# Optimization experiments

Measured on AMD Instinct MI355X. Metric: run time of the kernel, lower is better.

The kernel has to match this reference:

```python
import jax, jax.numpy as jnp
import numpy as np

B, S, E = 2, 2048, 1024
N_HEADS = 16
HEAD_DIM = E // N_HEADS  # 64
ATTN_SCALE = 1.0 / np.sqrt(E)  # NOTE: original scales by 1/sqrt(hidden_dim_phi), not head_dim
ROPE_BASE = 10000.0


def _rope(t):
    # t: (B, H, S, D) with D = HEAD_DIM; interleaved-pair RoPE (torchtune-style)
    d = t.shape[-1]
    s = t.shape[-2]
    inv_freq = 1.0 / (ROPE_BASE ** (jnp.arange(0, d, 2, dtype=jnp.float32) / d))  # (D/2,)
    ang = jnp.arange(s, dtype=jnp.float32)[:, None] * inv_freq[None, :]  # (S, D/2)
    cos, sin = jnp.cos(ang), jnp.sin(ang)  # (S, D/2)
    tp = t.reshape(t.shape[:-1] + (d // 2, 2))
    te, to = tp[..., 0], tp[..., 1]  # (B,H,S,D/2)
    oe = te * cos - to * sin
    oo = te * sin + to * cos
    return jnp.stack([oe, oo], axis=-1).reshape(t.shape)


def setup_inputs() -> dict:
    key = jax.random.key(0)
    ks = jax.random.split(key, 5)
    std = 0.02
    return {
        "x": jax.random.normal(ks[0], (B, S, E), dtype=jnp.float32),
        "W_q": jax.random.normal(ks[1], (E, E), dtype=jnp.float32) * std,
        "W_k": jax.random.normal(ks[2], (E, E), dtype=jnp.float32) * std,
        "W_v": jax.random.normal(ks[3], (E, E), dtype=jnp.float32) * std,
        "W_o": jax.random.normal(ks[4], (E, E), dtype=jnp.float32) * std,
    }


def reference(x, W_q, W_k, W_v, W_o):
    b, s, e = x.shape
    hd = e // N_HEADS
    # projections -> (B, H, S, D)
    def proj(w):
        return (x @ w).reshape(b, s, N_HEADS, hd).transpose(0, 2, 1, 3)
    q = _rope(proj(W_q))
    k = _rope(proj(W_k))
    v = proj(W_v)
    scores = jnp.einsum('bhsd,bhtd->bhst', q, k) * ATTN_SCALE  # (B,H,S,S)
    causal = jnp.triu(jnp.ones((s, s), dtype=bool), k=1)
    scores = jnp.where(causal, -jnp.inf, scores)
    probs = jax.nn.softmax(scores, axis=-1)  # dropout is identity in eval mode
    out = jnp.einsum('bhst,bhtd->bhsd', probs, v)
    out = out.transpose(0, 2, 1, 3).reshape(b, s, e)
    return out @ W_o
```

## Files before the change

### kernel.cpp

```cpp
#include <hip/hip_runtime.h>
#include <hip/hip_bf16.h>

#define S_LEN 2048
#define E_DIM 1024
#define NH 16
#define HD 64
#define ATTN_SCALE 0.03125f
#define QSCALE_L2E 0.045084312f

typedef __attribute__((ext_vector_type(8))) short short8;
typedef __attribute__((ext_vector_type(8))) unsigned short ushort8;
typedef __attribute__((ext_vector_type(4))) unsigned short ushort4_t;
typedef __attribute__((ext_vector_type(4))) float f32x4;
typedef __attribute__((ext_vector_type(16))) float f32x16;
typedef __attribute__((ext_vector_type(4))) float f4;
typedef __attribute__((ext_vector_type(4))) unsigned int uint4v;

__device__ __forceinline__ float bf2f(unsigned short u) {
    unsigned int x = ((unsigned int)u) << 16;
    return __builtin_bit_cast(float, x);
}
__device__ __forceinline__ unsigned short f2bf(float f) {
    unsigned int x = __builtin_bit_cast(unsigned int, f);
    x += 0x7FFFu + ((x >> 16) & 1u);
    return (unsigned short)(x >> 16);
}
__device__ __forceinline__ float exp2_fast(float x) {
    float r;
    asm("v_exp_f32 %0, %1" : "=v"(r) : "v"(x));
    return r;
}
__device__ __forceinline__ void gload16(const unsigned short* g, unsigned short* l) {
    __builtin_amdgcn_global_load_lds(
        (__attribute__((address_space(1))) void*)g,
        (__attribute__((address_space(3))) void*)l, 16, 0, 0);
}

__global__ __launch_bounds__(256) void k_convert(const float* __restrict__ x,
                                                 unsigned short* __restrict__ xb) {
    size_t i = ((size_t)blockIdx.x * 256 + threadIdx.x) * 8;
    f4 a = *(const f4*)(x + i);
    f4 b = *(const f4*)(x + i + 4);
    ushort8 o;
    o[0] = f2bf(a[0]); o[1] = f2bf(a[1]); o[2] = f2bf(a[2]); o[3] = f2bf(a[3]);
    o[4] = f2bf(b[0]); o[5] = f2bf(b[1]); o[6] = f2bf(b[2]); o[7] = f2bf(b[3]);
    *(ushort8*)(xb + i) = o;
}

__global__ __launch_bounds__(256) void k_transw(const float* W0, const float* W1,
                                                const float* W2, const float* W3,
                                                unsigned short* T0, unsigned short* T1,
                                                unsigned short* T2, unsigned short* T3) {
    const float* W; unsigned short* T;
    switch (blockIdx.z) {
        case 0: W = W0; T = T0; break;
        case 1: W = W1; T = T1; break;
        case 2: W = W2; T = T2; break;
        default: W = W3; T = T3; break;
    }
    __shared__ float tile[32][33];
    int tx = threadIdx.x, ty = threadIdx.y;
    int bx = blockIdx.x * 32, by = blockIdx.y * 32;
#pragma unroll
    for (int i = 0; i < 4; i++)
        tile[ty + i * 8][tx] = W[(size_t)(by + ty + i * 8) * E_DIM + bx + tx];
    __syncthreads();
#pragma unroll
    for (int i = 0; i < 4; i++)
        T[(size_t)(bx + ty + i * 8) * E_DIM + by + tx] = f2bf(tile[tx][ty + i * 8]);
}

__global__ __launch_bounds__(256) void k_rope_table(float* __restrict__ cosT,
                                                    float* __restrict__ sinT) {
    int idx = blockIdx.x * 256 + threadIdx.x;
    int s = idx >> 5, j = idx & 31;
    float inv = expf(-(float)j * (9.210340371976184f / 32.f));
    float ang = (float)s * inv;
    cosT[idx] = cosf(ang);
    sinT[idx] = sinf(ang);
}

template <int BM, int BN, int NBN, bool QKV3>
__global__ __launch_bounds__(256, 3)
void k_gemmN(const unsigned short* __restrict__ A,
             const unsigned short* __restrict__ B,
             unsigned short* __restrict__ Qo,
             unsigned short* __restrict__ Ko,
             unsigned short* __restrict__ Vto,
             float* __restrict__ Fo,
             const float* __restrict__ cosT,
             const float* __restrict__ sinT) {
    constexpr int THREADS = 256;
    constexpr int WM = BM / 2, WN = BN / 2;
    constexpr int FM = WM / 16, FN = WN / 16;
    constexpr int NT = E_DIM / 64;
    constexpr int AR = BM * 8 / THREADS;
    constexpr int BR = BN * 8 / THREADS;
    constexpr int STG = AR + BR;
    constexpr int NWG = (4096 / BM) * NBN;
    __shared__ unsigned short Al[2][BM * 64];
    __shared__ unsigned short Bl[2][BN * 64];
    int tid = threadIdx.x, lane = tid & 63, wid = tid >> 6;
    int l15 = lane & 15, lg = lane >> 4;
    int wr = wid >> 1, wc = wid & 1;
    int orig = blockIdx.y * NBN + blockIdx.x;
    int wg = (orig & 7) * (NWG / 8) + (orig >> 3);
    int bm = wg / NBN, bn = wg % NBN;

    auto stage = [&](int buf, int k0) {
#pragma unroll
        for (int i = 0; i < AR; i++) {
            int r = i * (THREADS / 8) + wid * 8 + (lane >> 3);
            int cs = (lane & 7) ^ (r & 7);
            gload16(A + (size_t)(bm * BM + r) * E_DIM + k0 + cs * 8,
                    &Al[buf][i * (THREADS * 8) + wid * 512]);
        }
#pragma unroll
        for (int i = 0; i < BR; i++) {
            int r = i * (THREADS / 8) + wid * 8 + (lane >> 3);
            int cs = (lane & 7) ^ (r & 7);
            gload16(B + (size_t)(bn * BN + r) * E_DIM + k0 + cs * 8,
                    &Bl[buf][i * (THREADS * 8) + wid * 512]);
        }
    };

    f32x4 acc[FM][FN] = {};
    stage(0, 0);
    for (int t = 0; t < NT; t++) {
        int cur = t & 1;
        if (t + 1 < NT) {
            stage(cur ^ 1, (t + 1) * 64);
            asm volatile("s_waitcnt vmcnt(%0)" :: "n"(STG) : "memory");
        } else {
            asm volatile("s_waitcnt vmcnt(0)" ::: "memory");
        }
        __builtin_amdgcn_s_barrier();
        __builtin_amdgcn_sched_barrier(0);
#pragma unroll
        for (int ks = 0; ks < 2; ks++) {
            short8 af[FM], bfv[FN];
#pragma unroll
            for (int m = 0; m < FM; m++) {
                int r = wr * WM + m * 16 + l15;
                int gc = ks * 4 + lg;
                af[m] = *(const short8*)&Al[cur][r * 64 + ((gc ^ (r & 7)) << 3)];
            }
#pragma unroll
            for (int n = 0; n < FN; n++) {
                int r = wc * WN + n * 16 + l15;
                int gc = ks * 4 + lg;
                bfv[n] = *(const short8*)&Bl[cur][r * 64 + ((gc ^ (r & 7)) << 3)];
            }
            __builtin_amdgcn_s_setprio(1);
#pragma unroll
            for (int m = 0; m < FM; m++)
#pragma unroll
                for (int n = 0; n < FN; n++)
                    acc[m][n] = __builtin_amdgcn_mfma_f32_16x16x32_bf16(
                        af[m], bfv[n], acc[m][n], 0, 0, 0);
            __builtin_amdgcn_s_setprio(0);
        }
        __builtin_amdgcn_s_barrier();
    }
#pragma unroll
    for (int m = 0; m < FM; m++) {
        int r0 = bm * BM + wr * WM + m * 16 + lg * 4;
#pragma unroll
        for (int n = 0; n < FN; n++) {
            int colg = bn * BN + wc * WN + n * 16 + l15;
            if (QKV3) {
                int z = colg >> 10, c1 = colg & 1023;
                if (z == 2) {
                    int h = c1 >> 6, d = c1 & 63;
                    int bb = r0 >> 11, s = r0 & 2047;
                    ushort4_t p;
#pragma unroll
                    for (int r = 0; r < 4; r++) p[r] = f2bf(acc[m][n][r]);
                    *(ushort4_t*)(Vto + (((size_t)((bb * 16 + h) * 64 + d)) << 11) + s) = p;
                } else {
                    unsigned short* T = z ? Ko : Qo;
                    int dl = c1 & 63, j = dl >> 1;
                    float sgn = (dl & 1) ? 1.f : -1.f;
                    float scq = z ? 1.f : QSCALE_L2E;
#pragma unroll
                    for (int r = 0; r < 4; r++) {
                        int row = r0 + r, s = row & 2047;
                        float c = cosT[s * 32 + j], sn = sinT[s * 32 + j];
                        float v = acc[m][n][r];
                        float p = __shfl_xor(v, 1);
                        T[(size_t)row * E_DIM + c1] = f2bf((v * c + sgn * p * sn) * scq);
                    }
                }
            } else {
#pragma unroll
                for (int r = 0; r < 4; r++)
                    Fo[(size_t)(r0 + r) * E_DIM + colg] = acc[m][n][r];
            }
        }
    }
}

__global__ __launch_bounds__(128, 2)
void k_attn32(const unsigned short* __restrict__ Q,
              const unsigned short* __restrict__ K,
              const unsigned short* __restrict__ Vt,
              unsigned short* __restrict__ O) {
    __shared__ unsigned short K_lds[2][4096];
    __shared__ unsigned short V_lds[2][4096];
    int tid = threadIdx.x, lane = tid & 63, wid = tid >> 6;
    int l31 = lane & 31, hi = lane >> 5;
    int orig = blockIdx.y * 32 + blockIdx.x;
    int xcd = orig & 7, idx = orig >> 3;
    int u = idx & 31, v = idx >> 5;
    int bh = xcd * 4 + v;
    int p = (v & 1) ? (31 - u) : u;
    int b = bh >> 4, h = bh & 15;
    const size_t base_qk = (size_t)b * S_LEN * E_DIM + (size_t)h * HD;
    const unsigned short* Vbh = Vt + ((size_t)(bh * 64) << 11);

    auto stageK = [&](int buf, int kt) {
#pragma unroll
        for (int i = 0; i < 4; i++) {
            int r = i * 16 + (tid >> 3);
            int cs = (tid & 7) ^ (r & 7);
            gload16(K + base_qk + (size_t)(kt * 64 + r) * E_DIM + cs * 8,
                    &K_lds[buf][i * 1024 + tid * 8]);
        }
    };
    auto stageV = [&](int buf, int kt) {
#pragma unroll
        for (int i = 0; i < 4; i++) {
            int r = i * 16 + (tid >> 3);
            int cs = (tid & 7) ^ (r & 7);
            gload16(Vbh + (size_t)r * 2048 + kt * 64 + cs * 8,
                    &V_lds[buf][i * 1024 + tid * 8]);
        }
    };

    int q_glob = p * 64 + wid * 32 + l31;
    const unsigned short* Qb = Q + base_qk + (size_t)q_glob * E_DIM;
    short8 qf[4];
#pragma unroll
    for (int s = 0; s < 4; s++)
        qf[s] = *(const short8*)(Qb + s * 16 + hi * 8);

    f32x16 ot0 = {}, ot1 = {};
    float m_i = -1e30f, l_i = 0.f;
    int nkt = p + 1;
    int swz = l31 & 7;
    stageK(0, 0);
    stageV(0, 0);
    asm volatile("s_waitcnt vmcnt(0)" ::: "memory");
    __builtin_amdgcn_s_barrier();
    __builtin_amdgcn_sched_barrier(0);
    int cur = 0;
    for (int kt = 0; kt < nkt; ++kt) {
        if (kt + 1 < nkt) {
            stageK(cur ^ 1, kt + 1);
            stageV(cur ^ 1, kt + 1);
        }
        f32x16 st0 = {}, st1 = {};
        __builtin_amdgcn_s_setprio(1);
#pragma unroll
        for (int s = 0; s < 4; s++) {
            int c = ((s * 2 + hi) ^ swz) << 3;
            short8 ka0 = *(const short8*)&K_lds[cur][l31 * 64 + c];
            short8 ka1 = *(const short8*)&K_lds[cur][(32 + l31) * 64 + c];
            st0 = __builtin_amdgcn_mfma_f32_32x32x16_bf16(ka0, qf[s], st0, 0, 0, 0);
            st1 = __builtin_amdgcn_mfma_f32_32x32x16_bf16(ka1, qf[s], st1, 0, 0, 0);
        }
        __builtin_amdgcn_s_setprio(0);
        float p0[16], p1[16];
        float vmax = -1e30f;
        if (kt == nkt - 1) {
#pragma unroll
            for (int r = 0; r < 16; r++) {
                int kg = kt * 64 + (r & 3) + 8 * (r >> 2) + 4 * hi;
                float v0 = (kg > q_glob) ? -1e30f : st0[r];
                float v1 = (kg + 32 > q_glob) ? -1e30f : st1[r];
                p0[r] = v0; p1[r] = v1;
                vmax = fmaxf(vmax, fmaxf(v0, v1));
            }
        } else {
#pragma unroll
            for (int r = 0; r < 16; r++) {
                p0[r] = st0[r]; p1[r] = st1[r];
                vmax = fmaxf(vmax, fmaxf(st0[r], st1[r]));
            }
        }
        vmax = fmaxf(vmax, __shfl_xor(vmax, 32));
        float m_new = fmaxf(m_i, vmax);
        float corr = exp2_fast(m_i - m_new);
        float rs = 0.f;
#pragma unroll
        for (int r = 0; r < 16; r++) {
            p0[r] = exp2_fast(p0[r] - m_new);
            p1[r] = exp2_fast(p1[r] - m_new);
            rs += p0[r] + p1[r];
        }
        rs += __shfl_xor(rs, 32);
        l_i = l_i * corr + rs;
        m_i = m_new;
#pragma unroll
        for (int r = 0; r < 16; r++) { ot0[r] *= corr; ot1[r] *= corr; }
        unsigned int pk0[8], pk1[8];
#pragma unroll
        for (int i = 0; i < 8; i++) {
            asm("v_cvt_pk_bf16_f32 %0, %1, %2"
                : "=v"(pk0[i]) : "v"(p0[2 * i]), "v"(p0[2 * i + 1]));
            asm("v_cvt_pk_bf16_f32 %0, %1, %2"
                : "=v"(pk1[i]) : "v"(p1[2 * i]), "v"(p1[2 * i + 1]));
        }
        bool ishi = hi != 0;
        __builtin_amdgcn_s_setprio(1);
#pragma unroll
        for (int kk = 0; kk < 4; kk++) {
            const unsigned int* pkt = (kk & 2) ? pk1 : pk0;
            int off = (kk & 1) * 4;
            unsigned int a  = pkt[off + 0], b2 = pkt[off + 1];
            unsigned int c2 = pkt[off + 2], d2 = pkt[off + 3];
            unsigned int sa = __shfl_xor(a, 32),  sb = __shfl_xor(b2, 32);
            unsigned int sc = __shfl_xor(c2, 32), sd = __shfl_xor(d2, 32);
            uint4v w;
            w[0] = ishi ? sc : a;  w[1] = ishi ? sd : b2;
            w[2] = ishi ? c2 : sa; w[3] = ishi ? d2 : sb;
            short8 pf = __builtin_bit_cast(short8, w);
            int cv = ((kk * 2 + hi) ^ swz) << 3;
            short8 va0 = *(const short8*)&V_lds[cur][l31 * 64 + cv];
            short8 va1 = *(const short8*)&V_lds[cur][(32 + l31) * 64 + cv];
            ot0 = __builtin_amdgcn_mfma_f32_32x32x16_bf16(va0, pf, ot0, 0, 0, 0);
            ot1 = __builtin_amdgcn_mfma_f32_32x32x16_bf16(va1, pf, ot1, 0, 0, 0);
        }
        __builtin_amdgcn_s_setprio(0);
        asm volatile("s_waitcnt vmcnt(0)" ::: "memory");
        __builtin_amdgcn_s_barrier();
        __builtin_amdgcn_sched_barrier(0);
        cur ^= 1;
    }
    __builtin_amdgcn_s_barrier();
    float linv = 1.f / l_i;
    unsigned short* scb = &K_lds[0][0] + wid * 2304;
#pragma unroll
    for (int i = 0; i < 8; i++) {
        int d = 2 * (i & 1) + 8 * (i >> 1) + 4 * hi;
        unsigned int w0, w1;
        float a0 = ot0[2 * i] * linv, a1 = ot0[2 * i + 1] * linv;
        float b0 = ot1[2 * i] * linv, b1 = ot1[2 * i + 1] * linv;
        asm("v_cvt_pk_bf16_f32 %0, %1, %2" : "=v"(w0) : "v"(a0), "v"(a1));
        asm("v_cvt_pk_bf16_f32 %0, %1, %2" : "=v"(w1) : "v"(b0), "v"(b1));
        *(unsigned int*)&scb[l31 * 72 + d] = w0;
        *(unsigned int*)&scb[l31 * 72 + 32 + d] = w1;
    }
    asm volatile("s_waitcnt lgkmcnt(0)" ::: "memory");
    __builtin_amdgcn_sched_barrier(0);
    int qr = lane >> 1, half = (lane & 1) * 32;
    unsigned short* Ob = O + base_qk + (size_t)(p * 64 + wid * 32 + qr) * E_DIM;
#pragma unroll
    for (int j = 0; j < 4; j++) {
        short8 vv = *(const short8*)&scb[qr * 72 + half + j * 8];
        *(short8*)(Ob + half + j * 8) = vv;
    }
}

extern "C" void kernel_launch(void* const* d_in, const int* in_sizes, int n_in,
                              void* d_out, int out_size, void* d_ws, size_t ws_size,
                              hipStream_t stream) {
    (void)in_sizes; (void)n_in; (void)out_size; (void)ws_size;
    const float* x  = (const float*)d_in[0];
    const float* Wq = (const float*)d_in[1];
    const float* Wk = (const float*)d_in[2];
    const float* Wv = (const float*)d_in[3];
    const float* Wo = (const float*)d_in[4];

    unsigned short* us = (unsigned short*)d_ws;
    unsigned short* xb    = us;
    unsigned short* WqkvT = us + 4194304;
    unsigned short* WoT   = us + 7340032;
    unsigned short* Qb    = us + 8388608;
    unsigned short* Kb    = us + 12582912;
    unsigned short* Vt    = us + 16777216;
    unsigned short* AO    = us + 20971520;
    float* cosT = (float*)((char*)d_ws + 50331648);
    float* sinT = cosT + 65536;

    k_convert<<<2048, 256, 0, stream>>>(x, xb);
    k_transw<<<dim3(32, 32, 4), dim3(32, 8), 0, stream>>>(
        Wq, Wk, Wv, Wo, WqkvT, WqkvT + 1048576, WqkvT + 2097152, WoT);
    k_rope_table<<<256, 256, 0, stream>>>(cosT, sinT);
    k_gemmN<128, 64, 48, true><<<dim3(48, 32), 256, 0, stream>>>(
        xb, WqkvT, Qb, Kb, Vt, nullptr, cosT, sinT);
    k_attn32<<<dim3(32, 32), 128, 0, stream>>>(Qb, Kb, Vt, AO);
    k_gemmN<128, 64, 16, false><<<dim3(16, 32), 256, 0, stream>>>(
        AO, WoT, nullptr, nullptr, nullptr, (float*)d_out, cosT, sinT);
}
```

Baseline: 117.7 us.

## Pre-pack K/V in MFMA fragment order and load attention operands straight from global

The QKV GEMM epilogue now writes K and V into a tiled layout that matches the 32x32x16 MFMA operand fragments per 64-key tile. The attention kernel becomes a single-wave, 32-query block that loads K/V fragments directly from global memory into registers with contiguous 16-byte loads, dropping LDS staging, swizzling, double buffering and barriers. This removes LDS traffic and sync, and gives the scheduler smaller blocks to balance the causal work. In exchange, K/V reuse across waves in a block is lost, so global/L2 traffic roughly doubles. Load latency is also no longer hidden by explicit prefetch, and the K epilogue now does scattered 2-byte stores.

```diff
diff --git a/kernel.cpp b/kernel.cpp
--- a/kernel.cpp
+++ b/kernel.cpp
@@ -170,25 +170,48 @@
             int colg = bn * BN + wc * WN + n * 16 + l15;
             if (QKV3) {
                 int z = colg >> 10, c1 = colg & 1023;
+                int dl = c1 & 63;
+                int bh2 = ((r0 >> 11) << 4) + (c1 >> 6);
                 if (z == 2) {
-                    int h = c1 >> 6, d = c1 & 63;
-                    int bb = r0 >> 11, s = r0 & 2047;
-                    ushort4_t p;
-#pragma unroll
-                    for (int r = 0; r < 4; r++) p[r] = f2bf(acc[m][n][r]);
-                    *(ushort4_t*)(Vto + (((size_t)((bb * 16 + h) * 64 + d)) << 11) + s) = p;
+                    int sq = r0 & 2047;
+                    int kt = sq >> 6, sr = sq & 63;
+                    int ks = sr >> 4, hiv = (sr >> 3) & 1, jv = sr & 7;
+                    int gp = dl >> 5, l31v = dl & 31;
+                    size_t off = (size_t)(bh2 * 32 + kt) * 4096 +
+                                 (size_t)(gp * 4 + ks) * 512 +
+                                 (size_t)(hiv * 32 + l31v) * 8 + jv;
+                    ushort4_t pv;
+#pragma unroll
+                    for (int r = 0; r < 4; r++) pv[r] = f2bf(acc[m][n][r]);
+                    *(ushort4_t*)(Vto + off) = pv;
+                } else if (z == 1) {
+                    int j = dl >> 1;
+                    float sgn = (dl & 1) ? 1.f : -1.f;
+                    int sk = dl >> 4, hik = (dl >> 3) & 1, jk = dl & 7;
+#pragma unroll
+                    for (int r = 0; r < 4; r++) {
+                        int row = r0 + r, sq = row & 2047;
+                        float c = cosT[sq * 32 + j], sn = sinT[sq * 32 + j];
+                        float v = acc[m][n][r];
+                        float pp = __shfl_xor(v, 1);
+                        float val = v * c + sgn * pp * sn;
+                        int kt = sq >> 6, rr = sq & 63;
+                        size_t off = (size_t)(bh2 * 32 + kt) * 4096 +
+                                     (size_t)(((rr >> 5) << 2) + sk) * 512 +
+                                     (size_t)(hik * 32 + (rr & 31)) * 8 + jk;
+                        Ko[off] = f2bf(val);
+                    }
                 } else {
-                    unsigned short* T = z ? Ko : Qo;
-                    int dl = c1 & 63, j = dl >> 1;
+                    int j = dl >> 1;
                     float sgn = (dl & 1) ? 1.f : -1.f;
-                    float scq = z ? 1.f : QSCALE_L2E;
 #pragma unroll
                     for (int r = 0; r < 4; r++) {
-                        int row = r0 + r, s = row & 2047;
-                        float c = cosT[s * 32 + j], sn = sinT[s * 32 + j];
+                        int row = r0 + r, sq = row & 2047;
+                        float c = cosT[sq * 32 + j], sn = sinT[sq * 32 + j];
                         float v = acc[m][n][r];
-                        float p = __shfl_xor(v, 1);
-                        T[(size_t)row * E_DIM + c1] = f2bf((v * c + sgn * p * sn) * scq);
+                        float pp = __shfl_xor(v, 1);
+                        Qo[(size_t)row * E_DIM + c1] =
+                            f2bf((v * c + sgn * pp * sn) * QSCALE_L2E);
                     }
                 }
             } else {
@@ -200,45 +223,26 @@
     }
 }
 
-__global__ __launch_bounds__(128, 2)
-void k_attn32(const unsigned short* __restrict__ Q,
-              const unsigned short* __restrict__ K,
-              const unsigned short* __restrict__ Vt,
-              unsigned short* __restrict__ O) {
-    __shared__ unsigned short K_lds[2][4096];
-    __shared__ unsigned short V_lds[2][4096];
-    int tid = threadIdx.x, lane = tid & 63, wid = tid >> 6;
+__global__ __launch_bounds__(64, 3)
+void k_attn32g(const unsigned short* __restrict__ Q,
+               const unsigned short* __restrict__ KP,
+               const unsigned short* __restrict__ VP,
+               unsigned short* __restrict__ O) {
+    __shared__ unsigned short scb[32 * 72];
+    int lane = threadIdx.x & 63;
     int l31 = lane & 31, hi = lane >> 5;
-    int orig = blockIdx.y * 32 + blockIdx.x;
+    int orig = blockIdx.y * 64 + blockIdx.x;
     int xcd = orig & 7, idx = orig >> 3;
-    int u = idx & 31, v = idx >> 5;
+    int v = idx & 3, u = idx >> 2;
     int bh = xcd * 4 + v;
-    int p = (v & 1) ? (31 - u) : u;
+    int p = (v & 1) ? (63 - u) : u;
     int b = bh >> 4, h = bh & 15;
-    const size_t base_qk = (size_t)b * S_LEN * E_DIM + (size_t)h * HD;
-    const unsigned short* Vbh = Vt + ((size_t)(bh * 64) << 11);
-
-    auto stageK = [&](int buf, int kt) {
-#pragma unroll
-        for (int i = 0; i < 4; i++) {
-            int r = i * 16 + (tid >> 3);
-            int cs = (tid & 7) ^ (r & 7);
-            gload16(K + base_qk + (size_t)(kt * 64 + r) * E_DIM + cs * 8,
-                    &K_lds[buf][i * 1024 + tid * 8]);
-        }
-    };
-    auto stageV = [&](int buf, int kt) {
-#pragma unroll
-        for (int i = 0; i < 4; i++) {
-            int r = i * 16 + (tid >> 3);
-            int cs = (tid & 7) ^ (r & 7);
-            gload16(Vbh + (size_t)r * 2048 + kt * 64 + cs * 8,
-                    &V_lds[buf][i * 1024 + tid * 8]);
-        }
-    };
-
-    int q_glob = p * 64 + wid * 32 + l31;
-    const unsigned short* Qb = Q + base_qk + (size_t)q_glob * E_DIM;
+    const size_t base_o = (size_t)b * S_LEN * E_DIM + (size_t)h * HD;
+    const unsigned short* KPb = KP + (size_t)bh * 32 * 4096;
+    const unsigned short* VPb = VP + (size_t)bh * 32 * 4096;
+
+    int q_glob = p * 32 + l31;
+    const unsigned short* Qb = Q + base_o + (size_t)q_glob * E_DIM;
     short8 qf[4];
 #pragma unroll
     for (int s = 0; s < 4; s++)
@@ -246,30 +250,30 @@
 
     f32x16 ot0 = {}, ot1 = {};
     float m_i = -1e30f, l_i = 0.f;
-    int nkt = p + 1;
-    int swz = l31 & 7;
-    stageK(0, 0);
-    stageV(0, 0);
-    asm volatile("s_waitcnt vmcnt(0)" ::: "memory");
-    __builtin_amdgcn_s_barrier();
-    __builtin_amdgcn_sched_barrier(0);
-    int cur = 0;
+    int nkt = (p >> 1) + 1;
     for (int kt = 0; kt < nkt; ++kt) {
-        if (kt + 1 < nkt) {
-            stageK(cur ^ 1, kt + 1);
-            stageV(cur ^ 1, kt + 1);
+        const unsigned short* kb = KPb + (size_t)kt * 4096;
+        const unsigned short* vb = VPb + (size_t)kt * 4096;
+        short8 ka0[4], ka1[4];
+#pragma unroll
+        for (int s = 0; s < 4; s++) {
+            ka0[s] = *(const short8*)(kb + s * 512 + lane * 8);
+            ka1[s] = *(const short8*)(kb + (4 + s) * 512 + lane * 8);
         }
         f32x16 st0 = {}, st1 = {};
         __builtin_amdgcn_s_setprio(1);
 #pragma unroll
         for (int s = 0; s < 4; s++) {
-            int c = ((s * 2 + hi) ^ swz) << 3;
-            short8 ka0 = *(const short8*)&K_lds[cur][l31 * 64 + c];
-            short8 ka1 = *(const short8*)&K_lds[cur][(32 + l31) * 64 + c];
-            st0 = __builtin_amdgcn_mfma_f32_32x32x16_bf16(ka0, qf[s], st0, 0, 0, 0);
-            st1 = __builtin_amdgcn_mfma_f32_32x32x16_bf16(ka1, qf[s], st1, 0, 0, 0);
+            st0 = __builtin_amdgcn_mfma_f32_32x32x16_bf16(ka0[s], qf[s], st0, 0, 0, 0);
+            st1 = __builtin_amdgcn_mfma_f32_32x32x16_bf16(ka1[s], qf[s], st1, 0, 0, 0);
         }
         __builtin_amdgcn_s_setprio(0);
+        short8 va0[4], va1[4];
+#pragma unroll
+        for (int s = 0; s < 4; s++) {
+            va0[s] = *(const short8*)(vb + s * 512 + lane * 8);
+            va1[s] = *(const short8*)(vb + (4 + s) * 512 + lane * 8);
+        }
         float p0[16], p1[16];
         float vmax = -1e30f;
         if (kt == nkt - 1) {
@@ -325,21 +329,12 @@
             w[0] = ishi ? sc : a;  w[1] = ishi ? sd : b2;
             w[2] = ishi ? c2 : sa; w[3] = ishi ? d2 : sb;
             short8 pf = __builtin_bit_cast(short8, w);
-            int cv = ((kk * 2 + hi) ^ swz) << 3;
-            short8 va0 = *(const short8*)&V_lds[cur][l31 * 64 + cv];
-            short8 va1 = *(const short8*)&V_lds[cur][(32 + l31) * 64 + cv];
-            ot0 = __builtin_amdgcn_mfma_f32_32x32x16_bf16(va0, pf, ot0, 0, 0, 0);
-            ot1 = __builtin_amdgcn_mfma_f32_32x32x16_bf16(va1, pf, ot1, 0, 0, 0);
+            ot0 = __builtin_amdgcn_mfma_f32_32x32x16_bf16(va0[kk], pf, ot0, 0, 0, 0);
+            ot1 = __builtin_amdgcn_mfma_f32_32x32x16_bf16(va1[kk], pf, ot1, 0, 0, 0);
         }
         __builtin_amdgcn_s_setprio(0);
-        asm volatile("s_waitcnt vmcnt(0)" ::: "memory");
-        __builtin_amdgcn_s_barrier();
-        __builtin_amdgcn_sched_barrier(0);
-        cur ^= 1;
-    }
-    __builtin_amdgcn_s_barrier();
+    }
     float linv = 1.f / l_i;
-    unsigned short* scb = &K_lds[0][0] + wid * 2304;
 #pragma unroll
     for (int i = 0; i < 8; i++) {
         int d = 2 * (i & 1) + 8 * (i >> 1) + 4 * hi;
@@ -354,7 +349,7 @@
     asm volatile("s_waitcnt lgkmcnt(0)" ::: "memory");
     __builtin_amdgcn_sched_barrier(0);
     int qr = lane >> 1, half = (lane & 1) * 32;
-    unsigned short* Ob = O + base_qk + (size_t)(p * 64 + wid * 32 + qr) * E_DIM;
+    unsigned short* Ob = O + base_o + (size_t)(p * 32 + qr) * E_DIM;
 #pragma unroll
     for (int j = 0; j < 4; j++) {
         short8 vv = *(const short8*)&scb[qr * 72 + half + j * 8];
@@ -377,8 +372,8 @@
     unsigned short* WqkvT = us + 4194304;
     unsigned short* WoT   = us + 7340032;
     unsigned short* Qb    = us + 8388608;
-    unsigned short* Kb    = us + 12582912;
-    unsigned short* Vt    = us + 16777216;
+    unsigned short* KP    = us + 12582912;
+    unsigned short* VP    = us + 16777216;
     unsigned short* AO    = us + 20971520;
     float* cosT = (float*)((char*)d_ws + 50331648);
     float* sinT = cosT + 65536;
@@ -388,8 +383,8 @@
         Wq, Wk, Wv, Wo, WqkvT, WqkvT + 1048576, WqkvT + 2097152, WoT);
     k_rope_table<<<256, 256, 0, stream>>>(cosT, sinT);
     k_gemmN<128, 64, 48, true><<<dim3(48, 32), 256, 0, stream>>>(
-        xb, WqkvT, Qb, Kb, Vt, nullptr, cosT, sinT);
-    k_attn32<<<dim3(32, 32), 128, 0, stream>>>(Qb, Kb, Vt, AO);
+        xb, WqkvT, Qb, KP, VP, nullptr, cosT, sinT);
+    k_attn32g<<<dim3(64, 32), 64, 0, stream>>>(Qb, KP, VP, AO);
     k_gemmN<128, 64, 16, false><<<dim3(16, 32), 256, 0, stream>>>(
         AO, WoT, nullptr, nullptr, nullptr, (float*)d_out, cosT, sinT);
 }
```

New measurement: 110.6 us. -6.0%, faster.
